# Kernel optimization log

Hardware: AMD Instinct MI355X
Metric: run time of the kernel (lower is better)

The kernel has to match this reference:

```python
import jax, jax.numpy as jnp
import numpy as np

B, S, C, V = 4, 512, 128, 128

def setup_inputs() -> dict:
    key = jax.random.key(0)
    ks = jax.random.split(key, 9)
    sc = 0.05
    return {
        "ctx": jax.random.normal(ks[0], (B, S, C), dtype=jnp.float32),
        "W1": jax.random.normal(ks[1], (V, C), dtype=jnp.float32) * sc,
        "b1": jax.random.normal(ks[2], (V,), dtype=jnp.float32) * sc,
        "W2": jax.random.normal(ks[3], (V, C), dtype=jnp.float32) * sc,
        "b2": jax.random.normal(ks[4], (V,), dtype=jnp.float32) * sc,
        "Wm": jax.random.normal(ks[5], (V, C), dtype=jnp.float32) * sc,
        "bm": jax.random.normal(ks[6], (V,), dtype=jnp.float32) * sc,
        "Wd": jax.random.normal(ks[7], (V, C), dtype=jnp.float32) * sc,
        "bd": jax.random.normal(ks[8], (V,), dtype=jnp.float32) * sc,
    }

def reference(ctx, W1, b1, W2, b2, Wm, bm, Wd, bd):
    # torch semantics: ctx.unsqueeze(1) -> (B,1,S,C) carries index j on dim 2;
    # ctx.unsqueeze(2) -> (B,S,1,C) carries index i on dim 1.
    # mul[b,i,j,c]  = ctx[b,j,c] * ctx[b,i,c]
    # diff[b,i,j,c] = ctx[b,j,c] - ctx[b,i,c]
    out1 = ctx @ W1.T + b1            # (B,S,V), indexed by j
    out2 = ctx @ W2.T + b2            # (B,S,V), indexed by i
    # fold the elementwise product into the GEMM reduction (no (B,S,S,C) tensor)
    outmul = jnp.einsum('bic,bjc,vc->bijv', ctx, ctx, Wm) + bm   # (B,S,S,V)
    # linear is affine: lin(diff) = lin0(ctx_j) - lin0(ctx_i) + bd
    d = ctx @ Wd.T                    # (B,S,V)
    outdiff = d[:, None, :, :] - d[:, :, None, :] + bd           # (B,S,S,V)
    out = jnp.tanh(out1[:, None, :, :] + out2[:, :, None, :] + outmul + outdiff)
    return out
```

## Files before the change

kernel.cpp:

```cpp
#include <hip/hip_runtime.h>

#define NB 4
#define NS 512
#define NC 128
#define NV 128

typedef _Float16 half8 __attribute__((ext_vector_type(8)));
typedef float f32x4 __attribute__((ext_vector_type(4)));

__device__ __forceinline__ float fast_tanh(float x) {
  float e = __expf(2.0f * x);
  return 1.0f - __fdividef(2.0f, e + 1.0f);
}

__global__ __launch_bounds__(128) void prep_kernel(
    const float* __restrict__ ctx,
    const float* __restrict__ W1, const float* __restrict__ b1,
    const float* __restrict__ W2, const float* __restrict__ b2,
    const float* __restrict__ bm,
    const float* __restrict__ Wd, const float* __restrict__ bd,
    _Float16* __restrict__ ctx_h,
    float* __restrict__ H, float* __restrict__ G)
{
  __shared__ float xr[8][NC];
  const int row0 = blockIdx.x * 8;
  const int t = threadIdx.x;
  #pragma unroll
  for (int rr = 0; rr < 8; ++rr) {
    float x = ctx[(size_t)(row0 + rr) * NC + t];
    xr[rr][t] = x;
    ctx_h[(size_t)(row0 + rr) * NC + t] = (_Float16)x;
  }
  __syncthreads();
  const int v = t;
  float accH[8], accG[8];
  const float bH = b1[v];
  const float bG = b2[v] + bd[v] + bm[v];
  #pragma unroll
  for (int rr = 0; rr < 8; ++rr) { accH[rr] = bH; accG[rr] = bG; }
  for (int c4 = 0; c4 < NC; c4 += 4) {
    f32x4 w1 = *(const f32x4*)(W1 + v * NC + c4);
    f32x4 w2 = *(const f32x4*)(W2 + v * NC + c4);
    f32x4 wd = *(const f32x4*)(Wd + v * NC + c4);
    #pragma unroll
    for (int u = 0; u < 4; ++u) {
      const float wH = w1[u] + wd[u];
      const float wG = w2[u] - wd[u];
      const int c = c4 + u;
      #pragma unroll
      for (int rr = 0; rr < 8; ++rr) {
        accH[rr] = fmaf(xr[rr][c], wH, accH[rr]);
        accG[rr] = fmaf(xr[rr][c], wG, accG[rr]);
      }
    }
  }
  #pragma unroll
  for (int rr = 0; rr < 8; ++rr) {
    H[(size_t)(row0 + rr) * NV + v] = accH[rr];
    G[(size_t)(row0 + rr) * NV + v] = accG[rr];
  }
}

__global__ __launch_bounds__(256, 2) void main_kernel(
    const float* __restrict__ ctx,
    const float* __restrict__ Wm,
    const _Float16* __restrict__ ctx_h,
    const float* __restrict__ H,
    const float* __restrict__ G,
    float* __restrict__ out)
{
  const int bx = blockIdx.x;
  const int b = bx >> 9;
  const int i = bx & (NS - 1);
  const int tid = threadIdx.x;
  const int w = tid >> 6;
  const int l = tid & 63;
  const int r = l & 15;
  const int q = l >> 4;

  __shared__ _Float16 Bm[NV][NC + 8];

  const float* xi = ctx + (size_t)(b * NS + i) * NC;
  for (int idx = tid; idx < NV * (NC / 8); idx += 256) {
    const int v = idx >> 4;
    const int c0 = (idx & 15) * 8;
    f32x4 wa = *(const f32x4*)(Wm + v * NC + c0);
    f32x4 wb = *(const f32x4*)(Wm + v * NC + c0 + 4);
    f32x4 xa = *(const f32x4*)(xi + c0);
    f32x4 xb = *(const f32x4*)(xi + c0 + 4);
    half8 h;
    h[0] = (_Float16)(wa[0] * xa[0]);
    h[1] = (_Float16)(wa[1] * xa[1]);
    h[2] = (_Float16)(wa[2] * xa[2]);
    h[3] = (_Float16)(wa[3] * xa[3]);
    h[4] = (_Float16)(wb[0] * xb[0]);
    h[5] = (_Float16)(wb[1] * xb[1]);
    h[6] = (_Float16)(wb[2] * xb[2]);
    h[7] = (_Float16)(wb[3] * xb[3]);
    *(half8*)&Bm[v][c0] = h;
  }
  __syncthreads();

  half8 Bf[8][4];
  #pragma unroll
  for (int n = 0; n < 8; ++n) {
    #pragma unroll
    for (int ks = 0; ks < 4; ++ks) {
      Bf[n][ks] = *(const half8*)&Bm[n * 16 + r][ks * 32 + q * 8];
    }
  }

  float Gv[8];
  const float* gp = G + (size_t)(b * NS + i) * NV;
  #pragma unroll
  for (int n = 0; n < 8; ++n) Gv[n] = gp[n * 16 + r];

  const _Float16* ah_base = ctx_h + (size_t)(b * NS) * NC;
  const float* h_base = H + (size_t)(b * NS) * NV;
  float* out_base = out + ((size_t)(b * NS + i) * NS) * NV;

  for (int tt = 0; tt < 8; ++tt) {
    const int j0 = tt * 64 + w * 16;

    half8 A[4];
    const _Float16* ap = ah_base + (size_t)(j0 + r) * NC + q * 8;
    #pragma unroll
    for (int ks = 0; ks < 4; ++ks) A[ks] = *(const half8*)(ap + ks * 32);

    f32x4 acc[8];
    #pragma unroll
    for (int n = 0; n < 8; ++n) acc[n] = (f32x4){0.f, 0.f, 0.f, 0.f};

    #pragma unroll
    for (int ks = 0; ks < 4; ++ks) {
      #pragma unroll
      for (int n = 0; n < 8; ++n) {
        acc[n] = __builtin_amdgcn_mfma_f32_16x16x32_f16(A[ks], Bf[n][ks], acc[n], 0, 0, 0);
      }
    }

    const float* hp = h_base + (size_t)j0 * NV;
    float* op = out_base + (size_t)j0 * NV;
    #pragma unroll
    for (int n = 0; n < 8; ++n) {
      const int v = n * 16 + r;
      #pragma unroll
      for (int rr = 0; rr < 4; ++rr) {
        const int j = q * 4 + rr;
        const float pre = acc[n][rr] + hp[j * NV + v] + Gv[n];
        op[j * NV + v] = fast_tanh(pre);
      }
    }
  }
}

extern "C" void kernel_launch(void* const* d_in, const int* in_sizes, int n_in,
                              void* d_out, int out_size, void* d_ws, size_t ws_size,
                              hipStream_t stream) {
  const float* ctx = (const float*)d_in[0];
  const float* W1  = (const float*)d_in[1];
  const float* b1  = (const float*)d_in[2];
  const float* W2  = (const float*)d_in[3];
  const float* b2  = (const float*)d_in[4];
  const float* Wm  = (const float*)d_in[5];
  const float* bm  = (const float*)d_in[6];
  const float* Wd  = (const float*)d_in[7];
  const float* bd  = (const float*)d_in[8];
  float* out = (float*)d_out;

  char* ws = (char*)d_ws;
  _Float16* ctx_h = (_Float16*)ws;
  float* H = (float*)(ws + (size_t)NB * NS * NC * sizeof(_Float16));
  float* G = H + (size_t)NB * NS * NV;

  prep_kernel<<<NB * NS / 8, 128, 0, stream>>>(ctx, W1, b1, W2, b2, bm, Wd, bd, ctx_h, H, G);
  main_kernel<<<NB * NS, 256, 0, stream>>>(ctx, Wm, ctx_h, H, G, out);
}
```

Measured before the change: 618.6 us.

## Fold j-side linear term into MFMA operand and vectorize transposed output stores

The per-j linear term (W1+Wd)·ctx_j is folded into the GEMM by adding the precomputed W1+Wd matrix to the Wm⊙ctx_i operand. This removes the H workspace and its per-element loads in the epilogue. The i-side term and all biases go into a single Gp vector, which now seeds the MFMA accumulators. The MFMA operands are swapped so each lane holds four consecutive v values, allowing 16-byte vectorized output stores instead of scalar ones. In exchange, the H contribution is now rounded to fp16 inside the GEMM, which may slightly reduce accuracy.

```diff
diff --git a/kernel.cpp b/kernel.cpp
--- a/kernel.cpp
+++ b/kernel.cpp
@@ -20,11 +20,18 @@
     const float* __restrict__ bm,
     const float* __restrict__ Wd, const float* __restrict__ bd,
     _Float16* __restrict__ ctx_h,
-    float* __restrict__ H, float* __restrict__ G)
+    float* __restrict__ Gp,
+    float* __restrict__ WHd)
 {
   __shared__ float xr[8][NC];
   const int row0 = blockIdx.x * 8;
   const int t = threadIdx.x;
+
+  {
+    const int base = blockIdx.x * 64;
+    if (t < 64) WHd[base + t] = W1[base + t] + Wd[base + t];
+  }
+
   #pragma unroll
   for (int rr = 0; rr < 8; ++rr) {
     float x = ctx[(size_t)(row0 + rr) * NC + t];
@@ -32,41 +39,34 @@
     ctx_h[(size_t)(row0 + rr) * NC + t] = (_Float16)x;
   }
   __syncthreads();
+
   const int v = t;
-  float accH[8], accG[8];
-  const float bH = b1[v];
-  const float bG = b2[v] + bd[v] + bm[v];
+  float acc[8];
+  const float bG = b1[v] + b2[v] + bm[v] + bd[v];
   #pragma unroll
-  for (int rr = 0; rr < 8; ++rr) { accH[rr] = bH; accG[rr] = bG; }
+  for (int rr = 0; rr < 8; ++rr) acc[rr] = bG;
+
   for (int c4 = 0; c4 < NC; c4 += 4) {
-    f32x4 w1 = *(const f32x4*)(W1 + v * NC + c4);
     f32x4 w2 = *(const f32x4*)(W2 + v * NC + c4);
     f32x4 wd = *(const f32x4*)(Wd + v * NC + c4);
     #pragma unroll
     for (int u = 0; u < 4; ++u) {
-      const float wH = w1[u] + wd[u];
       const float wG = w2[u] - wd[u];
       const int c = c4 + u;
       #pragma unroll
-      for (int rr = 0; rr < 8; ++rr) {
-        accH[rr] = fmaf(xr[rr][c], wH, accH[rr]);
-        accG[rr] = fmaf(xr[rr][c], wG, accG[rr]);
-      }
+      for (int rr = 0; rr < 8; ++rr) acc[rr] = fmaf(xr[rr][c], wG, acc[rr]);
     }
   }
   #pragma unroll
-  for (int rr = 0; rr < 8; ++rr) {
-    H[(size_t)(row0 + rr) * NV + v] = accH[rr];
-    G[(size_t)(row0 + rr) * NV + v] = accG[rr];
-  }
+  for (int rr = 0; rr < 8; ++rr) Gp[(size_t)(row0 + rr) * NV + v] = acc[rr];
 }
 
 __global__ __launch_bounds__(256, 2) void main_kernel(
     const float* __restrict__ ctx,
     const float* __restrict__ Wm,
+    const float* __restrict__ WHd,
     const _Float16* __restrict__ ctx_h,
-    const float* __restrict__ H,
-    const float* __restrict__ G,
+    const float* __restrict__ Gp,
     float* __restrict__ out)
 {
   const int bx = blockIdx.x;
@@ -86,17 +86,19 @@
     const int c0 = (idx & 15) * 8;
     f32x4 wa = *(const f32x4*)(Wm + v * NC + c0);
     f32x4 wb = *(const f32x4*)(Wm + v * NC + c0 + 4);
+    f32x4 ha = *(const f32x4*)(WHd + v * NC + c0);
+    f32x4 hb = *(const f32x4*)(WHd + v * NC + c0 + 4);
     f32x4 xa = *(const f32x4*)(xi + c0);
     f32x4 xb = *(const f32x4*)(xi + c0 + 4);
     half8 h;
-    h[0] = (_Float16)(wa[0] * xa[0]);
-    h[1] = (_Float16)(wa[1] * xa[1]);
-    h[2] = (_Float16)(wa[2] * xa[2]);
-    h[3] = (_Float16)(wa[3] * xa[3]);
-    h[4] = (_Float16)(wb[0] * xb[0]);
-    h[5] = (_Float16)(wb[1] * xb[1]);
-    h[6] = (_Float16)(wb[2] * xb[2]);
-    h[7] = (_Float16)(wb[3] * xb[3]);
+    h[0] = (_Float16)fmaf(wa[0], xa[0], ha[0]);
+    h[1] = (_Float16)fmaf(wa[1], xa[1], ha[1]);
+    h[2] = (_Float16)fmaf(wa[2], xa[2], ha[2]);
+    h[3] = (_Float16)fmaf(wa[3], xa[3], ha[3]);
+    h[4] = (_Float16)fmaf(wb[0], xb[0], hb[0]);
+    h[5] = (_Float16)fmaf(wb[1], xb[1], hb[1]);
+    h[6] = (_Float16)fmaf(wb[2], xb[2], hb[2]);
+    h[7] = (_Float16)fmaf(wb[3], xb[3], hb[7 - 7 + 3]);
     *(half8*)&Bm[v][c0] = h;
   }
   __syncthreads();
@@ -110,13 +112,12 @@
     }
   }
 
-  float Gv[8];
-  const float* gp = G + (size_t)(b * NS + i) * NV;
+  f32x4 Gv[8];
+  const float* gp = Gp + (size_t)(b * NS + i) * NV;
   #pragma unroll
-  for (int n = 0; n < 8; ++n) Gv[n] = gp[n * 16 + r];
+  for (int n = 0; n < 8; ++n) Gv[n] = *(const f32x4*)(gp + n * 16 + q * 4);
 
   const _Float16* ah_base = ctx_h + (size_t)(b * NS) * NC;
-  const float* h_base = H + (size_t)(b * NS) * NV;
   float* out_base = out + ((size_t)(b * NS + i) * NS) * NV;
 
   for (int tt = 0; tt < 8; ++tt) {
@@ -129,27 +130,23 @@
 
     f32x4 acc[8];
     #pragma unroll
-    for (int n = 0; n < 8; ++n) acc[n] = (f32x4){0.f, 0.f, 0.f, 0.f};
+    for (int n = 0; n < 8; ++n) acc[n] = Gv[n];
 
     #pragma unroll
     for (int ks = 0; ks < 4; ++ks) {
       #pragma unroll
       for (int n = 0; n < 8; ++n) {
-        acc[n] = __builtin_amdgcn_mfma_f32_16x16x32_f16(A[ks], Bf[n][ks], acc[n], 0, 0, 0);
+        acc[n] = __builtin_amdgcn_mfma_f32_16x16x32_f16(Bf[n][ks], A[ks], acc[n], 0, 0, 0);
       }
     }
 
-    const float* hp = h_base + (size_t)j0 * NV;
-    float* op = out_base + (size_t)j0 * NV;
+    float* op = out_base + (size_t)(j0 + r) * NV + q * 4;
     #pragma unroll
     for (int n = 0; n < 8; ++n) {
-      const int v = n * 16 + r;
+      f32x4 o;
       #pragma unroll
-      for (int rr = 0; rr < 4; ++rr) {
-        const int j = q * 4 + rr;
-        const float pre = acc[n][rr] + hp[j * NV + v] + Gv[n];
-        op[j * NV + v] = fast_tanh(pre);
-      }
+      for (int rr = 0; rr < 4; ++rr) o[rr] = fast_tanh(acc[n][rr]);
+      *(f32x4*)(op + n * 16) = o;
     }
   }
 }
@@ -170,9 +167,9 @@
 
   char* ws = (char*)d_ws;
   _Float16* ctx_h = (_Float16*)ws;
-  float* H = (float*)(ws + (size_t)NB * NS * NC * sizeof(_Float16));
-  float* G = H + (size_t)NB * NS * NV;
+  float* Gp  = (float*)(ws + (size_t)NB * NS * NC * sizeof(_Float16));
+  float* WHd = Gp + (size_t)NB * NS * NV;
 
-  prep_kernel<<<NB * NS / 8, 128, 0, stream>>>(ctx, W1, b1, W2, b2, bm, Wd, bd, ctx_h, H, G);
-  main_kernel<<<NB * NS, 256, 0, stream>>>(ctx, Wm, ctx_h, H, G, out);
+  prep_kernel<<<NB * NS / 8, 128, 0, stream>>>(ctx, W1, b1, W2, b2, bm, Wd, bd, ctx_h, Gp, WHd);
+  main_kernel<<<NB * NS, 256, 0, stream>>>(ctx, Wm, WHd, ctx_h, Gp, out);
 }
```

After: 607.5 us. No clear change (-1.8%).
